# Kernel tuning notes

Measured on AMD Instinct MI355X. Metric: run time of the kernel, lower is better.

## Reference

```python
import jax, jax.numpy as jnp
import numpy as np

N = 8192  # source points
M = 8192  # target points
T = 8     # RL path steps


def setup_inputs() -> dict:
    key = jax.random.key(0)
    ks = jax.random.split(key, 6)
    return {
        "source": jax.random.normal(ks[0], (N, 3), jnp.float32),
        "target": jax.random.normal(ks[1], (M, 3), jnp.float32),
        "label": jax.random.uniform(ks[2], (N,), jnp.float32),
        "trans_m": 0.01 * jax.random.normal(ks[3], (T, N, 3), jnp.float32),
        "path_m": jax.random.uniform(ks[4], (T, N), jnp.float32),
        "path_maxprob_m": jax.random.uniform(ks[5], (T, N), jnp.float32, minval=0.05, maxval=1.0),
    }


def _catculate_loss2(p1, p2):
    # p1: [N,3], p2: [M,3] -> pairwise squared distances [N,M]
    dist = jnp.sum((p1[:, None, :] - p2[None, :, :]) ** 2, axis=-1)
    dist_min = jnp.min(dist, axis=-1)
    dist_max = jnp.max(dist, axis=-1)
    return 0.99 * dist_min + 0.01 * dist_max  # [N]


def reference(source, target, label, trans_m, path_m, path_maxprob_m):
    p = 0.002
    L0 = 0.4
    lammda = 0.05
    gamma = 0.99
    Tn = path_m.shape[0]

    trans_end = trans_m[-1]
    points_denoise = source - trans_end
    loss_start = _catculate_loss2(source, target)
    loss_end = _catculate_loss2(points_denoise, target)
    loss_dt = loss_end - loss_start

    d = jnp.minimum(loss_end / L0, 1.0)  # where(d>1, 1, d)
    l = jnp.exp(-label)

    reward_end = -p * path_m[-1] - (d + lammda * l) * loss_dt  # [N]
    # rewards: [N, T] = per-step path penalties then final reward
    rewards = jnp.concatenate([(-p * path_m[:-1]).T, reward_end[:, None]], axis=-1)

    logp = jnp.log(path_maxprob_m)  # [T, N]

    # discounted return scan, iterating i = T-1 .. 0
    def step(carry, xs):
        R, L = carry
        lp, r = xs
        R = gamma * R + lp * (r + 0.02)
        return (R, L - R), None

    init = (jnp.zeros_like(reward_end), jnp.zeros_like(reward_end))
    (_, L), _ = jax.lax.scan(step, init, (logp[::-1], rewards.T[::-1]))
    loss = L / Tn  # [N]
    return jnp.mean(loss)
```

## Files before the change

kernel.cpp:

```cpp
#include <hip/hip_runtime.h>
#include <math.h>

#define TPB 256
#define TILE 128

__global__ __launch_bounds__(TPB) void k1_partial_minmax(
    const float* __restrict__ source,
    const float* __restrict__ target,
    const float* __restrict__ trans_m,
    float4* __restrict__ part,
    int* __restrict__ counter,
    int N, int M, int T, int S)
{
    if (blockIdx.x == 0 && blockIdx.y == 0 && threadIdx.x == 0) *counter = 0;

    const int chunk = M / S;
    const int i = blockIdx.x * TPB + threadIdx.x;
    const int s = blockIdx.y;

    __shared__ float4 tgt[TILE];

    const float sx = source[i * 3 + 0];
    const float sy = source[i * 3 + 1];
    const float sz = source[i * 3 + 2];
    const long teoff = (long)(T - 1) * N * 3 + (long)i * 3;
    const float ex = sx - trans_m[teoff + 0];
    const float ey = sy - trans_m[teoff + 1];
    const float ez = sz - trans_m[teoff + 2];

    const float ss = fmaf(sx, sx, fmaf(sy, sy, sz * sz));
    const float ee = fmaf(ex, ex, fmaf(ey, ey, ez * ez));
    const float vsx = -2.0f * sx, vsy = -2.0f * sy, vsz = -2.0f * sz;
    const float vex = -2.0f * ex, vey = -2.0f * ey, vez = -2.0f * ez;

    float mins = 3.402823e38f, maxs = -3.402823e38f;
    float mine = 3.402823e38f, maxe = -3.402823e38f;

    const int t_begin = s * chunk;
    const int t_end   = t_begin + chunk;

    for (int t0 = t_begin; t0 < t_end; t0 += TILE) {
        __syncthreads();
        for (int j = threadIdx.x; j < TILE; j += TPB) {
            const float tx = target[(long)(t0 + j) * 3 + 0];
            const float ty = target[(long)(t0 + j) * 3 + 1];
            const float tz = target[(long)(t0 + j) * 3 + 2];
            const float q  = fmaf(tx, tx, fmaf(ty, ty, tz * tz));
            tgt[j] = make_float4(tx, ty, tz, q);
        }
        __syncthreads();

        #pragma unroll 8
        for (int j = 0; j < TILE; ++j) {
            const float4 t = tgt[j];
            float a = fmaf(vsx, t.x, t.w);
            a = fmaf(vsy, t.y, a);
            a = fmaf(vsz, t.z, a);
            mins = fminf(mins, a);
            maxs = fmaxf(maxs, a);
            float b = fmaf(vex, t.x, t.w);
            b = fmaf(vey, t.y, b);
            b = fmaf(vez, t.z, b);
            mine = fminf(mine, b);
            maxe = fmaxf(maxe, b);
        }
    }

    part[(long)s * N + i] = make_float4(mins + ss, maxs + ss, mine + ee, maxe + ee);
}

__global__ __launch_bounds__(TPB) void k2_loss(
    const float4* __restrict__ part,
    const float* __restrict__ label,
    const float* __restrict__ path_m,
    const float* __restrict__ path_maxprob_m,
    float* __restrict__ blocksums,
    int* __restrict__ counter,
    float* __restrict__ out,
    int N, int S, int T)
{
    const int i = blockIdx.x * TPB + threadIdx.x;

    float mins = 3.402823e38f, maxs = -3.402823e38f;
    float mine = 3.402823e38f, maxe = -3.402823e38f;
    #pragma unroll 4
    for (int s = 0; s < S; ++s) {
        const float4 v = part[(long)s * N + i];
        mins = fminf(mins, v.x);
        maxs = fmaxf(maxs, v.y);
        mine = fminf(mine, v.z);
        maxe = fmaxf(maxe, v.w);
    }

    const float p = 0.002f, L0 = 0.4f, lam = 0.05f, gamma = 0.99f;
    const float loss_start = 0.99f * mins + 0.01f * maxs;
    const float loss_end   = 0.99f * mine + 0.01f * maxe;
    const float loss_dt    = loss_end - loss_start;
    const float d = fminf(loss_end / L0, 1.0f);
    const float l = expf(-label[i]);
    const float reward_end = -p * path_m[(long)(T - 1) * N + i]
                             - (d + lam * l) * loss_dt;

    float R = 0.0f, L = 0.0f;
    for (int t = T - 1; t >= 0; --t) {
        const float r  = (t == T - 1) ? reward_end
                                      : (-p * path_m[(long)t * N + i]);
        const float lp = logf(path_maxprob_m[(long)t * N + i]);
        R = gamma * R + lp * (r + 0.02f);
        L -= R;
    }
    float v = L / (float)T;

    for (int off = 32; off > 0; off >>= 1) v += __shfl_down(v, off, 64);
    __shared__ float red[TPB / 64];
    __shared__ bool amLast;
    const int wid = threadIdx.x >> 6, lane = threadIdx.x & 63;
    if (lane == 0) red[wid] = v;
    __syncthreads();
    if (threadIdx.x == 0) {
        float t = 0.0f;
        #pragma unroll
        for (int w = 0; w < TPB / 64; ++w) t += red[w];
        blocksums[blockIdx.x] = t;
        __threadfence();
        const int old = atomicAdd(counter, 1);
        amLast = (old == (int)gridDim.x - 1);
    }
    __syncthreads();
    if (amLast && threadIdx.x == 0) {
        __threadfence();
        float tot = 0.0f;
        for (int b = 0; b < (int)gridDim.x; ++b)
            tot += ((volatile float*)blocksums)[b];
        out[0] = tot / (float)N;
    }
}

extern "C" void kernel_launch(void* const* d_in, const int* in_sizes, int n_in,
                              void* d_out, int out_size, void* d_ws, size_t ws_size,
                              hipStream_t stream) {
    const float* source = (const float*)d_in[0];
    const float* target = (const float*)d_in[1];
    const float* label  = (const float*)d_in[2];
    const float* trans  = (const float*)d_in[3];
    const float* path   = (const float*)d_in[4];
    const float* pmax   = (const float*)d_in[5];

    const int N = in_sizes[0] / 3;
    const int M = in_sizes[1] / 3;
    const int T = in_sizes[3] / (N * 3);
    const int nbx = N / TPB;

    int S = 64;
    while (S > 1 && ((size_t)S * N * sizeof(float4)
                         + (size_t)(nbx + 1) * sizeof(float) > ws_size
                     || (M / S) < TILE))
        S >>= 1;

    float4* part     = (float4*)d_ws;
    float* blocksums = (float*)(part + (size_t)S * N);
    int*   counter   = (int*)(blocksums + nbx);

    k1_partial_minmax<<<dim3(nbx, S), TPB, 0, stream>>>(
        source, target, trans, part, counter, N, M, T, S);
    k2_loss<<<nbx, TPB, 0, stream>>>(
        part, label, path, pmax, blocksums, counter, (float*)d_out, N, S, T);
}
```

Baseline: 88.61 us.

## Process two source points per thread in min/max kernel and shrink loss blocks

Each thread in the distance kernel now handles two source points, so every target float4 read from shared memory is reused across two points. This cuts LDS traffic per FMA and halves the number of x-blocks, at the cost of more registers. The loss kernel moves to 64-thread blocks, dropping the shared-memory cross-wave reduction, and the final blocksum reduction is now done in parallel by the last block's wavefront. With fewer blocks in the first kernel (16x64 = 1024), occupancy on the GPU may be lower.

```diff
diff --git a/kernel.cpp b/kernel.cpp
--- a/kernel.cpp
+++ b/kernel.cpp
@@ -2,7 +2,9 @@
 #include <math.h>
 
 #define TPB 256
+#define SPT 2
 #define TILE 128
+#define TPB2 64
 
 __global__ __launch_bounds__(TPB) void k1_partial_minmax(
     const float* __restrict__ source,
@@ -15,26 +17,33 @@
     if (blockIdx.x == 0 && blockIdx.y == 0 && threadIdx.x == 0) *counter = 0;
 
     const int chunk = M / S;
-    const int i = blockIdx.x * TPB + threadIdx.x;
     const int s = blockIdx.y;
+    const int i0 = blockIdx.x * (TPB * SPT) + threadIdx.x;
 
     __shared__ float4 tgt[TILE];
 
-    const float sx = source[i * 3 + 0];
-    const float sy = source[i * 3 + 1];
-    const float sz = source[i * 3 + 2];
-    const long teoff = (long)(T - 1) * N * 3 + (long)i * 3;
-    const float ex = sx - trans_m[teoff + 0];
-    const float ey = sy - trans_m[teoff + 1];
-    const float ez = sz - trans_m[teoff + 2];
+    float vsx[SPT], vsy[SPT], vsz[SPT];
+    float vex[SPT], vey[SPT], vez[SPT];
+    float ss[SPT], ee[SPT];
+    float mins[SPT], maxs[SPT], mine[SPT], maxe[SPT];
 
-    const float ss = fmaf(sx, sx, fmaf(sy, sy, sz * sz));
-    const float ee = fmaf(ex, ex, fmaf(ey, ey, ez * ez));
-    const float vsx = -2.0f * sx, vsy = -2.0f * sy, vsz = -2.0f * sz;
-    const float vex = -2.0f * ex, vey = -2.0f * ey, vez = -2.0f * ez;
-
-    float mins = 3.402823e38f, maxs = -3.402823e38f;
-    float mine = 3.402823e38f, maxe = -3.402823e38f;
+    #pragma unroll
+    for (int k = 0; k < SPT; ++k) {
+        const int i = i0 + k * TPB;
+        const float sx = source[(long)i * 3 + 0];
+        const float sy = source[(long)i * 3 + 1];
+        const float sz = source[(long)i * 3 + 2];
+        const long teoff = (long)(T - 1) * N * 3 + (long)i * 3;
+        const float ex = sx - trans_m[teoff + 0];
+        const float ey = sy - trans_m[teoff + 1];
+        const float ez = sz - trans_m[teoff + 2];
+        ss[k] = fmaf(sx, sx, fmaf(sy, sy, sz * sz));
+        ee[k] = fmaf(ex, ex, fmaf(ey, ey, ez * ez));
+        vsx[k] = -2.0f * sx; vsy[k] = -2.0f * sy; vsz[k] = -2.0f * sz;
+        vex[k] = -2.0f * ex; vey[k] = -2.0f * ey; vez[k] = -2.0f * ez;
+        mins[k] = 3.402823e38f; maxs[k] = -3.402823e38f;
+        mine[k] = 3.402823e38f; maxe[k] = -3.402823e38f;
+    }
 
     const int t_begin = s * chunk;
     const int t_end   = t_begin + chunk;
@@ -53,23 +62,31 @@
         #pragma unroll 8
         for (int j = 0; j < TILE; ++j) {
             const float4 t = tgt[j];
-            float a = fmaf(vsx, t.x, t.w);
-            a = fmaf(vsy, t.y, a);
-            a = fmaf(vsz, t.z, a);
-            mins = fminf(mins, a);
-            maxs = fmaxf(maxs, a);
-            float b = fmaf(vex, t.x, t.w);
-            b = fmaf(vey, t.y, b);
-            b = fmaf(vez, t.z, b);
-            mine = fminf(mine, b);
-            maxe = fmaxf(maxe, b);
+            #pragma unroll
+            for (int k = 0; k < SPT; ++k) {
+                float a = fmaf(vsx[k], t.x, t.w);
+                a = fmaf(vsy[k], t.y, a);
+                a = fmaf(vsz[k], t.z, a);
+                mins[k] = fminf(mins[k], a);
+                maxs[k] = fmaxf(maxs[k], a);
+                float b = fmaf(vex[k], t.x, t.w);
+                b = fmaf(vey[k], t.y, b);
+                b = fmaf(vez[k], t.z, b);
+                mine[k] = fminf(mine[k], b);
+                maxe[k] = fmaxf(maxe[k], b);
+            }
         }
     }
 
-    part[(long)s * N + i] = make_float4(mins + ss, maxs + ss, mine + ee, maxe + ee);
+    #pragma unroll
+    for (int k = 0; k < SPT; ++k) {
+        const int i = i0 + k * TPB;
+        part[(long)s * N + i] = make_float4(mins[k] + ss[k], maxs[k] + ss[k],
+                                            mine[k] + ee[k], maxe[k] + ee[k]);
+    }
 }
 
-__global__ __launch_bounds__(TPB) void k2_loss(
+__global__ __launch_bounds__(TPB2) void k2_loss(
     const float4* __restrict__ part,
     const float* __restrict__ label,
     const float* __restrict__ path_m,
@@ -79,11 +96,11 @@
     float* __restrict__ out,
     int N, int S, int T)
 {
-    const int i = blockIdx.x * TPB + threadIdx.x;
+    const int i = blockIdx.x * TPB2 + threadIdx.x;
 
     float mins = 3.402823e38f, maxs = -3.402823e38f;
     float mine = 3.402823e38f, maxe = -3.402823e38f;
-    #pragma unroll 4
+    #pragma unroll 8
     for (int s = 0; s < S; ++s) {
         const float4 v = part[(long)s * N + i];
         mins = fminf(mins, v.x);
@@ -112,27 +129,22 @@
     float v = L / (float)T;
 
     for (int off = 32; off > 0; off >>= 1) v += __shfl_down(v, off, 64);
-    __shared__ float red[TPB / 64];
+
     __shared__ bool amLast;
-    const int wid = threadIdx.x >> 6, lane = threadIdx.x & 63;
-    if (lane == 0) red[wid] = v;
-    __syncthreads();
     if (threadIdx.x == 0) {
-        float t = 0.0f;
-        #pragma unroll
-        for (int w = 0; w < TPB / 64; ++w) t += red[w];
-        blocksums[blockIdx.x] = t;
+        blocksums[blockIdx.x] = v;
         __threadfence();
         const int old = atomicAdd(counter, 1);
         amLast = (old == (int)gridDim.x - 1);
     }
     __syncthreads();
-    if (amLast && threadIdx.x == 0) {
+    if (amLast) {
         __threadfence();
-        float tot = 0.0f;
-        for (int b = 0; b < (int)gridDim.x; ++b)
-            tot += ((volatile float*)blocksums)[b];
-        out[0] = tot / (float)N;
+        float t = 0.0f;
+        for (int b = threadIdx.x; b < (int)gridDim.x; b += TPB2)
+            t += ((volatile float*)blocksums)[b];
+        for (int off = 32; off > 0; off >>= 1) t += __shfl_down(t, off, 64);
+        if (threadIdx.x == 0) out[0] = t / (float)N;
     }
 }
 
@@ -149,20 +161,21 @@
     const int N = in_sizes[0] / 3;
     const int M = in_sizes[1] / 3;
     const int T = in_sizes[3] / (N * 3);
-    const int nbx = N / TPB;
+    const int nbx  = N / (TPB * SPT);
+    const int nbx2 = N / TPB2;
 
     int S = 64;
     while (S > 1 && ((size_t)S * N * sizeof(float4)
-                         + (size_t)(nbx + 1) * sizeof(float) > ws_size
+                         + (size_t)(nbx2 + 1) * sizeof(float) > ws_size
                      || (M / S) < TILE))
         S >>= 1;
 
     float4* part     = (float4*)d_ws;
     float* blocksums = (float*)(part + (size_t)S * N);
-    int*   counter   = (int*)(blocksums + nbx);
+    int*   counter   = (int*)(blocksums + nbx2);
 
     k1_partial_minmax<<<dim3(nbx, S), TPB, 0, stream>>>(
         source, target, trans, part, counter, N, M, T, S);
-    k2_loss<<<nbx, TPB, 0, stream>>>(
+    k2_loss<<<nbx2, TPB2, 0, stream>>>(
         part, label, path, pmax, blocksums, counter, (float*)d_out, N, S, T);
 }
```

After: 87.60 us. About the same (-1.1%).
